# Kernel optimization log

Measured on AMD Instinct MI355X. Metric: run time of the kernel, lower is better.

Reference implementation:

```python
import jax, jax.numpy as jnp
import numpy as np

P = 8192      # num_pois
U = 4096      # num_users
E = 4096      # num directed hyperedges
D = 128       # emb_dim
B = 1024      # batch of user indices
T_UP = 1.0    # args.t1
T_GEO = 1.0   # args.t2
T_P2P = 1.0   # args.t3
ALPHA = 0.8   # constant alpha in Geo_ODEFunc


def setup_inputs() -> dict:
    key = jax.random.key(0)
    ks = jax.random.split(key, 13)
    return {
        "poi_emb_weight": jax.random.normal(ks[0], (P + 1, D), jnp.float32) * 0.02,
        "w_gate_geo": jax.random.normal(ks[1], (D, D), jnp.float32) * 0.05,
        "b_gate_geo": jax.random.normal(ks[2], (1, D), jnp.float32) * 0.05,
        "w_gate_seq": jax.random.normal(ks[3], (D, D), jnp.float32) * 0.05,
        "b_gate_seq": jax.random.normal(ks[4], (1, D), jnp.float32) * 0.05,
        "w_gate_col": jax.random.normal(ks[5], (D, D), jnp.float32) * 0.05,
        "b_gate_col": jax.random.normal(ks[6], (1, D), jnp.float32) * 0.05,
        "HG_up": jax.random.uniform(ks[7], (U, P), jnp.float32) * (1.0 / P),
        "HG_pu": jax.random.uniform(ks[8], (P, U), jnp.float32) * (1.0 / U),
        "HG_poi_src": jax.random.uniform(ks[9], (P, E), jnp.float32) * (1.0 / E),
        "HG_poi_tar": jax.random.uniform(ks[10], (E, P), jnp.float32) * (1.0 / P),
        "poi_geo_graph": jax.random.uniform(ks[11], (P, P), jnp.float32) * (1.0 / P),
        "user_idx": jax.random.randint(ks[12], (B,), 0, U, jnp.int32),
    }


def _gate(pe, w, b):
    # pois_embs * sigmoid(pois_embs @ W + b)
    return pe * jax.nn.sigmoid(pe @ w + b)


def reference(poi_emb_weight, w_gate_geo, b_gate_geo, w_gate_seq, b_gate_seq,
              w_gate_col, b_gate_col, HG_up, HG_pu, HG_poi_src, HG_poi_tar,
              poi_geo_graph, user_idx):
    pe = poi_emb_weight[:-1]                      # drop padding row -> [P, D]
    geo_gate = _gate(pe, w_gate_geo, b_gate_geo)
    seq_gate = _gate(pe, w_gate_seq, b_gate_seq)
    col_gate = _gate(pe, w_gate_col, b_gate_col)

    # U2P ODE, single Euler step on t=[0, T_UP]:
    #   f(x) = (HG_pu@HG_up - I)@x + e, e = x0; A@x factored to avoid [P,P].
    x = col_gate
    hg_pois = x + T_UP * (HG_pu @ (HG_up @ x) - x + x)

    # Geo ODE: f(x) = (alpha/2)*G@x - x + e, e = x0, alpha = 0.8.
    g = geo_gate
    geo_pois = g + T_GEO * ((ALPHA / 2.0) * (poi_geo_graph @ g) - g + g)

    # P2P (directed hypergraph) ODE: A = src@tar, f(x) = (A - I)@x + e.
    s = seq_gate
    trans_pois = s + T_P2P * (HG_poi_src @ (HG_poi_tar @ s) - s + s)

    # structural user embeddings, gathered at batch indices
    hg_users = (HG_up @ hg_pois)[user_idx]        # [B, D]
    geo_users = (HG_up @ geo_pois)[user_idx]      # [B, D]

    # [3P + 2B, D]
    return jnp.concatenate([hg_pois, geo_pois, trans_pois, hg_users, geo_users], axis=0)
```

## Files before the change

### kernel.cpp

```cpp
#include <hip/hip_runtime.h>
#include <hip/hip_bf16.h>

#define PP 8192
#define UU 4096
#define EE 4096
#define BB 1024

using f32x4  = __attribute__((ext_vector_type(4))) float;
using u32x4  = __attribute__((ext_vector_type(4))) unsigned int;
using bf16x8 = __attribute__((ext_vector_type(8))) short;
typedef __hip_bfloat16 bf16_t;

__device__ __forceinline__ unsigned cvt2(float a, float b){
  unsigned r;
  asm("v_cvt_pk_bf16_f32 %0, %1, %2" : "=v"(r) : "v"(a), "v"(b));
  return r;
}

__device__ __forceinline__ void gload16(const void* g, void* l){
  __builtin_amdgcn_global_load_lds((const __attribute__((address_space(1))) void*)g,
                                   (__attribute__((address_space(3))) void*)l, 16, 0, 0);
}

struct Job {
  const float*  A;
  const bf16_t* Bt;
  const float*  add;
  const float*  bvec;
  float*        outF;
  bf16_t*       outT;
  int           outTstride;
  float         scale;
  int           K;
  int           nb;
  int           mode;
};

#define BUFB 24576

__global__ __launch_bounds__(256, 2) void gemm_skinny(Job j0, Job j1, Job j2){
  __shared__ char smem[3*BUFB];
  int bid = blockIdx.x;
  Job j = j0;
  if (bid >= j.nb){ bid -= j.nb; j = j1; if (bid >= j.nb){ bid -= j.nb; j = j2; } }
  const int K = j.K;
  const int T = K >> 6;
  const int m0 = bid << 5;
  const int tid = threadIdx.x;
  const int lane = tid & 63;
  const int wid = tid >> 6;
  const int wm = wid >> 1, wk = wid & 1;

  const char* Ab = (const char*)j.A;
  const char* Bb = (const char*)j.Bt;

  size_t a_src[2]; unsigned a_lds[2];
  #pragma unroll
  for (int i = 0; i < 2; ++i){
    int row = wid*8 + i*4 + (lane>>4);
    int sb  = (lane & 15) << 4;
    a_src[i] = (size_t)(m0 + row)*(size_t)K*4 + (size_t)(sb ^ ((row & 15) << 4));
    a_lds[i] = (unsigned)((wid*8 + i*4) * 256);
  }
  size_t b_src[4]; unsigned b_lds[4];
  #pragma unroll
  for (int i = 0; i < 4; ++i){
    int n  = wid*32 + i*8 + (lane>>3);
    int sb = (lane & 7) << 4;
    b_src[i] = (size_t)n*(size_t)K*2 + (size_t)(sb ^ ((n & 7) << 4));
    b_lds[i] = (unsigned)(8192 + (wid*32 + i*8) * 128);
  }

  const int arow = wm*16 + (lane & 15);
  const unsigned acb  = (unsigned)(wk*128 + ((lane>>4) * 32));
  const unsigned aswz = (unsigned)((lane & 15) << 4);
  const unsigned a_rd0 = arow*256 + (acb ^ aswz);
  const unsigned a_rd1 = arow*256 + ((acb + 16) ^ aswz);
  unsigned b_rd[8];
  #pragma unroll
  for (int n0 = 0; n0 < 8; ++n0){
    int n = n0*16 + (lane & 15);
    unsigned c = (unsigned)(wk*64 + ((lane>>4) * 16));
    b_rd[n0] = 8192u + n*128 + (c ^ ((n & 7) << 4));
  }

  const f32x4 fzero = {0.f, 0.f, 0.f, 0.f};
  f32x4 acc[8];
  #pragma unroll
  for (int i = 0; i < 8; ++i) acc[i] = fzero;

  auto STAGE = [&](unsigned bufoff, int t){
    char* l = smem + bufoff;
    size_t ka = (size_t)t * 256;
    size_t kb = (size_t)t * 128;
    #pragma unroll
    for (int i = 0; i < 2; ++i) gload16(Ab + a_src[i] + ka, l + a_lds[i]);
    #pragma unroll
    for (int i = 0; i < 4; ++i) gload16(Bb + b_src[i] + kb, l + b_lds[i]);
  };

  STAGE(0, 0);
  if (T > 1){
    STAGE(BUFB, 1);
    asm volatile("s_waitcnt vmcnt(6)" ::: "memory");
  } else {
    asm volatile("s_waitcnt vmcnt(0)" ::: "memory");
  }
  __builtin_amdgcn_s_barrier();

  for (int t = 0; t < T; ++t){
    char* l = smem + (unsigned)(t % 3) * BUFB;
    if (t + 2 < T) STAGE((unsigned)((t+2) % 3) * BUFB, t + 2);
    f32x4 a0 = *(const f32x4*)(l + a_rd0);
    f32x4 a1 = *(const f32x4*)(l + a_rd1);
    union { bf16x8 v; unsigned u[4]; } af;
    af.u[0] = cvt2(a0.x, a0.y);
    af.u[1] = cvt2(a0.z, a0.w);
    af.u[2] = cvt2(a1.x, a1.y);
    af.u[3] = cvt2(a1.z, a1.w);
    #pragma unroll
    for (int n0 = 0; n0 < 8; ++n0){
      bf16x8 bfr = *(const bf16x8*)(l + b_rd[n0]);
      acc[n0] = __builtin_amdgcn_mfma_f32_16x16x32_bf16(af.v, bfr, acc[n0], 0, 0, 0);
    }
    if (t + 1 < T){
      if (t + 2 < T) asm volatile("s_waitcnt vmcnt(6)" ::: "memory");
      else           asm volatile("s_waitcnt vmcnt(0)" ::: "memory");
      __builtin_amdgcn_s_barrier();
    }
  }

  __syncthreads();
  float* red = (float*)smem;
  if (wk == 1){
    #pragma unroll
    for (int n0 = 0; n0 < 8; ++n0)
      #pragma unroll
      for (int q = 0; q < 4; ++q){
        int row = wm*16 + ((lane>>4)<<2) + q;
        int col = n0*16 + (lane & 15);
        red[row*128 + col] = acc[n0][q];
      }
  }
  __syncthreads();
  if (wk == 0){
    #pragma unroll
    for (int n0 = 0; n0 < 8; ++n0)
      #pragma unroll
      for (int q = 0; q < 4; ++q){
        int row = wm*16 + ((lane>>4)<<2) + q;
        int col = n0*16 + (lane & 15);
        float v = (acc[n0][q] + red[row*128 + col]) * j.scale;
        size_t gp = (size_t)(m0 + row);
        if (j.mode == 1){
          float pe = j.add[gp*128 + col];
          float bb = j.bvec[col];
          v = pe / (1.f + __expf(-(v + bb)));
        } else if (j.add){
          v += j.add[gp*128 + col];
        }
        acc[n0][q] = v;
        if (j.outF) j.outF[gp*128 + col] = v;
      }
  }

  if (j.outT){
    __syncthreads();
    if (wk == 0){
      #pragma unroll
      for (int n0 = 0; n0 < 8; ++n0)
        #pragma unroll
        for (int q = 0; q < 4; ++q){
          int row = wm*16 + ((lane>>4)<<2) + q;
          int col = n0*16 + (lane & 15);
          red[row*128 + col] = acc[n0][q];
        }
    }
    __syncthreads();
    int col = tid & 127, seg = tid >> 7;
    unsigned wrds[8] __attribute__((aligned(16)));
    #pragma unroll
    for (int r = 0; r < 8; ++r){
      float v0 = red[(seg*16 + 2*r    )*128 + col];
      float v1 = red[(seg*16 + 2*r + 1)*128 + col];
      wrds[r] = cvt2(v0, v1);
    }
    bf16_t* dst = j.outT + (size_t)col * (size_t)j.outTstride + (m0 + seg*16);
    *(u32x4*)dst       = *(const u32x4*)&wrds[0];
    *((u32x4*)dst + 1) = *(const u32x4*)&wrds[4];
  }
}

#define GBUFB 40960

__global__ __launch_bounds__(256, 1) void gemm_gather(const float* __restrict__ Aup,
    const int* __restrict__ uidx, const bf16_t* __restrict__ B5t, float* __restrict__ partials){
  __shared__ char smem[3*GBUFB];
  const int bid = blockIdx.x;
  const int mtile = bid & 31, split = bid >> 5;
  const int tid = threadIdx.x, lane = tid & 63, wid = tid >> 6;
  const int wm = wid >> 1, wk = wid & 1;
  const int T = 16;
  const char* Ab = (const char*)Aup;
  const char* Bb = (const char*)B5t;

  size_t a_src[2]; unsigned a_lds[2];
  #pragma unroll
  for (int i = 0; i < 2; ++i){
    int row  = wid*8 + i*4 + (lane>>4);
    int grow = uidx[mtile*32 + row];
    int sb   = (lane & 15) << 4;
    a_src[i] = (size_t)grow*(size_t)(PP*4) + (size_t)((sb ^ ((row & 15) << 4)) + split*4096);
    a_lds[i] = (unsigned)((wid*8 + i*4) * 256);
  }
  size_t b_src[8]; unsigned b_lds[8];
  #pragma unroll
  for (int i = 0; i < 8; ++i){
    int n  = wid*64 + i*8 + (lane>>3);
    int sb = (lane & 7) << 4;
    b_src[i] = (size_t)n*(size_t)(PP*2) + (size_t)((sb ^ ((n & 7) << 4)) + split*2048);
    b_lds[i] = (unsigned)(8192 + (wid*64 + i*8) * 128);
  }
  const int arow = wm*16 + (lane & 15);
  const unsigned acb  = (unsigned)(wk*128 + ((lane>>4)*32));
  const unsigned aswz = (unsigned)((lane & 15) << 4);
  const unsigned a_rd0 = arow*256 + (acb ^ aswz);
  const unsigned a_rd1 = arow*256 + ((acb + 16) ^ aswz);
  unsigned b_rd[16];
  #pragma unroll
  for (int n0 = 0; n0 < 16; ++n0){
    int n = n0*16 + (lane & 15);
    unsigned c = (unsigned)(wk*64 + ((lane>>4)*16));
    b_rd[n0] = 8192u + n*128 + (c ^ ((n & 7) << 4));
  }
  const f32x4 fzero = {0.f,0.f,0.f,0.f};
  f32x4 acc[16];
  #pragma unroll
  for (int i = 0; i < 16; ++i) acc[i] = fzero;

  auto STAGE = [&](unsigned bufoff, int t){
    char* l = smem + bufoff;
    size_t ka = (size_t)t*256, kb = (size_t)t*128;
    #pragma unroll
    for (int i = 0; i < 2; ++i) gload16(Ab + a_src[i] + ka, l + a_lds[i]);
    #pragma unroll
    for (int i = 0; i < 8; ++i) gload16(Bb + b_src[i] + kb, l + b_lds[i]);
  };
  STAGE(0, 0);
  STAGE(GBUFB, 1);
  asm volatile("s_waitcnt vmcnt(10)" ::: "memory");
  __builtin_amdgcn_s_barrier();
  for (int t = 0; t < T; ++t){
    char* l = smem + (unsigned)(t % 3) * GBUFB;
    if (t + 2 < T) STAGE((unsigned)((t+2)%3)*GBUFB, t+2);
    f32x4 a0 = *(const f32x4*)(l + a_rd0);
    f32x4 a1 = *(const f32x4*)(l + a_rd1);
    union { bf16x8 v; unsigned u[4]; } af;
    af.u[0] = cvt2(a0.x, a0.y);
    af.u[1] = cvt2(a0.z, a0.w);
    af.u[2] = cvt2(a1.x, a1.y);
    af.u[3] = cvt2(a1.z, a1.w);
    #pragma unroll
    for (int n0 = 0; n0 < 16; ++n0){
      bf16x8 bfr = *(const bf16x8*)(l + b_rd[n0]);
      acc[n0] = __builtin_amdgcn_mfma_f32_16x16x32_bf16(af.v, bfr, acc[n0], 0,0,0);
    }
    if (t + 1 < T){
      if (t + 2 < T) asm volatile("s_waitcnt vmcnt(10)" ::: "memory");
      else           asm volatile("s_waitcnt vmcnt(0)" ::: "memory");
      __builtin_amdgcn_s_barrier();
    }
  }
  __syncthreads();
  float* red = (float*)smem;
  if (wk == 1){
    #pragma unroll
    for (int n0 = 0; n0 < 16; ++n0)
      #pragma unroll
      for (int q = 0; q < 4; ++q){
        int row = wm*16 + ((lane>>4)<<2) + q;
        int col = n0*16 + (lane & 15);
        red[row*256 + col] = acc[n0][q];
      }
  }
  __syncthreads();
  if (wk == 0){
    #pragma unroll
    for (int n0 = 0; n0 < 16; ++n0)
      #pragma unroll
      for (int q = 0; q < 4; ++q){
        int row = wm*16 + ((lane>>4)<<2) + q;
        int col = n0*16 + (lane & 15);
        float v = acc[n0][q] + red[row*256 + col];
        partials[((size_t)split*1024 + mtile*32 + row)*256 + col] = v;
      }
  }
}

__global__ void prep_wt(const float* w0, const float* w1, const float* w2,
                        bf16_t* o0, bf16_t* o1, bf16_t* o2){
  const float* w = (blockIdx.x == 0) ? w0 : (blockIdx.x == 1) ? w1 : w2;
  bf16_t*      o = (blockIdx.x == 0) ? o0 : (blockIdx.x == 1) ? o1 : o2;
  int tid = threadIdx.x;
  int n = tid >> 1, h = tid & 1;
  unsigned wr[32] __attribute__((aligned(16)));
  #pragma unroll
  for (int r = 0; r < 32; ++r){
    float v0 = w[(h*64 + 2*r    )*128 + n];
    float v1 = w[(h*64 + 2*r + 1)*128 + n];
    wr[r] = cvt2(v0, v1);
  }
  u32x4* dst = (u32x4*)(o + n*128 + h*64);
  #pragma unroll
  for (int i = 0; i < 8; ++i) dst[i] = *(const u32x4*)&wr[i*4];
}

__global__ void reduce_users(const float* __restrict__ partials, float* __restrict__ out){
  int idx = blockIdx.x * 256 + threadIdx.x;
  int b = idx >> 8, n = idx & 255;
  float s = 0.f;
  #pragma unroll
  for (int k = 0; k < 8; ++k) s += partials[((size_t)k*1024 + b)*256 + n];
  if (n < 128) out[((size_t)(3*PP) + b)*128 + n]           = s;
  else         out[((size_t)(3*PP) + BB + b)*128 + (n-128)] = s;
}

extern "C" void kernel_launch(void* const* d_in, const int* in_sizes, int n_in,
                              void* d_out, int out_size, void* d_ws, size_t ws_size,
                              hipStream_t stream){
  const float* pe   = (const float*)d_in[0];
  const float* wgeo = (const float*)d_in[1];
  const float* bgeo = (const float*)d_in[2];
  const float* wseq = (const float*)d_in[3];
  const float* bseq = (const float*)d_in[4];
  const float* wcol = (const float*)d_in[5];
  const float* bcol = (const float*)d_in[6];
  const float* hup  = (const float*)d_in[7];
  const float* hpu  = (const float*)d_in[8];
  const float* hsrc = (const float*)d_in[9];
  const float* htar = (const float*)d_in[10];
  const float* geo  = (const float*)d_in[11];
  const int*   uidx = (const int*)d_in[12];
  float* out = (float*)d_out;

  char* w = (char*)d_ws;
  const size_t MB = 1024*1024;
  float*  x_f32 = (float*)(w);
  float*  g_f32 = (float*)(w + 4*MB);
  float*  s_f32 = (float*)(w + 8*MB);
  bf16_t* xT    = (bf16_t*)(w + 12*MB);
  bf16_t* gT    = (bf16_t*)(w + 14*MB);
  bf16_t* sT    = (bf16_t*)(w + 16*MB);
  bf16_t* upT   = (bf16_t*)(w + 18*MB);
  bf16_t* tarT  = (bf16_t*)(w + 19*MB);
  bf16_t* b5t   = (bf16_t*)(w + 20*MB);
  bf16_t* wtg   = (bf16_t*)(w + 24*MB);
  bf16_t* wts   = (bf16_t*)(w + 24*MB + 32768);
  bf16_t* wtc   = (bf16_t*)(w + 24*MB + 65536);
  float*  parts = (float*)(w + 25*MB);

  prep_wt<<<3, 256, 0, stream>>>(wgeo, wseq, wcol, wtg, wts, wtc);

  Job jg{pe, wtg, pe, bgeo, g_f32, gT, PP, 1.f, 128, 256, 1};
  Job js{pe, wts, pe, bseq, s_f32, sT, PP, 1.f, 128, 256, 1};
  Job jc{pe, wtc, pe, bcol, x_f32, xT, PP, 1.f, 128, 256, 1};
  gemm_skinny<<<768, 256, 0, stream>>>(jg, js, jc);

  Job j1 {hup,  xT, nullptr, nullptr, nullptr,               upT,                     UU, 1.f,  PP, 128, 0};
  Job j3 {geo,  gT, g_f32,   nullptr, out + (size_t)PP*128,  b5t + (size_t)128*PP,    PP, 0.4f, PP, 256, 0};
  Job j4a{htar, sT, nullptr, nullptr, nullptr,               tarT,                    EE, 1.f,  PP, 128, 0};
  gemm_skinny<<<512, 256, 0, stream>>>(j1, j3, j4a);

  Job j2 {hpu,  upT,  x_f32, nullptr, out,                     b5t,     PP, 1.f, UU, 256, 0};
  Job j4b{hsrc, tarT, s_f32, nullptr, out + (size_t)2*PP*128,  nullptr, 0,  1.f, EE, 256, 0};
  Job jd = j4b; jd.nb = 0;
  gemm_skinny<<<512, 256, 0, stream>>>(j2, j4b, jd);

  gemm_gather<<<256, 256, 0, stream>>>(hup, uidx, b5t, parts);
  reduce_users<<<1024, 256, 0, stream>>>(parts, out);
}
```

Baseline: 286.6 us.

## Double skinny GEMM block to 512 threads, splitting N across wave pairs

Changes gemm_skinny from 256 to 512 threads per block. The 8 waves are split by M, K-half and N-half, so each wave holds 4 accumulator tiles instead of 8 and issues fewer global-to-LDS loads per stage. The vmcnt waits and the transposed bf16 store are adjusted to match. The A-swizzle read uses arow instead of lane, which is equivalent here, in both kernels. The aim is more waves in flight to hide memory latency on these bandwidth-bound skinny GEMMs, at the cost of more barrier participants and higher launch-bounds occupancy demands against 72KB of LDS per block.

New measurement: 274.3 us. -4.3%, faster.

```diff
diff --git a/kernel.cpp b/kernel.cpp
--- a/kernel.cpp
+++ b/kernel.cpp
@@ -38,7 +38,7 @@
 
 #define BUFB 24576
 
-__global__ __launch_bounds__(256, 2) void gemm_skinny(Job j0, Job j1, Job j2){
+__global__ __launch_bounds__(512, 4) void gemm_skinny(Job j0, Job j1, Job j2){
   __shared__ char smem[3*BUFB];
   int bid = blockIdx.x;
   Job j = j0;
@@ -49,60 +49,60 @@
   const int tid = threadIdx.x;
   const int lane = tid & 63;
   const int wid = tid >> 6;
-  const int wm = wid >> 1, wk = wid & 1;
+  const int wn = wid & 1, wk = (wid >> 1) & 1, wm = wid >> 2;
 
   const char* Ab = (const char*)j.A;
   const char* Bb = (const char*)j.Bt;
 
-  size_t a_src[2]; unsigned a_lds[2];
+  size_t a_src; unsigned a_lds;
+  {
+    int L = wid;
+    int row = L*4 + (lane>>4);
+    int sb  = (lane & 15) << 4;
+    a_src = (size_t)(m0 + row)*(size_t)K*4 + (size_t)(sb ^ ((row & 15) << 4));
+    a_lds = (unsigned)(L * 1024);
+  }
+  size_t b_src[2]; unsigned b_lds[2];
   #pragma unroll
   for (int i = 0; i < 2; ++i){
-    int row = wid*8 + i*4 + (lane>>4);
-    int sb  = (lane & 15) << 4;
-    a_src[i] = (size_t)(m0 + row)*(size_t)K*4 + (size_t)(sb ^ ((row & 15) << 4));
-    a_lds[i] = (unsigned)((wid*8 + i*4) * 256);
-  }
-  size_t b_src[4]; unsigned b_lds[4];
-  #pragma unroll
-  for (int i = 0; i < 4; ++i){
-    int n  = wid*32 + i*8 + (lane>>3);
+    int L = wid*2 + i;
+    int n  = L*8 + (lane>>3);
     int sb = (lane & 7) << 4;
     b_src[i] = (size_t)n*(size_t)K*2 + (size_t)(sb ^ ((n & 7) << 4));
-    b_lds[i] = (unsigned)(8192 + (wid*32 + i*8) * 128);
+    b_lds[i] = (unsigned)(8192 + L * 1024);
   }
 
   const int arow = wm*16 + (lane & 15);
   const unsigned acb  = (unsigned)(wk*128 + ((lane>>4) * 32));
-  const unsigned aswz = (unsigned)((lane & 15) << 4);
+  const unsigned aswz = (unsigned)((arow & 15) << 4);
   const unsigned a_rd0 = arow*256 + (acb ^ aswz);
   const unsigned a_rd1 = arow*256 + ((acb + 16) ^ aswz);
-  unsigned b_rd[8];
-  #pragma unroll
-  for (int n0 = 0; n0 < 8; ++n0){
-    int n = n0*16 + (lane & 15);
+  unsigned b_rd[4];
+  #pragma unroll
+  for (int n0 = 0; n0 < 4; ++n0){
+    int n = wn*64 + n0*16 + (lane & 15);
     unsigned c = (unsigned)(wk*64 + ((lane>>4) * 16));
     b_rd[n0] = 8192u + n*128 + (c ^ ((n & 7) << 4));
   }
 
   const f32x4 fzero = {0.f, 0.f, 0.f, 0.f};
-  f32x4 acc[8];
-  #pragma unroll
-  for (int i = 0; i < 8; ++i) acc[i] = fzero;
+  f32x4 acc[4];
+  #pragma unroll
+  for (int i = 0; i < 4; ++i) acc[i] = fzero;
 
   auto STAGE = [&](unsigned bufoff, int t){
     char* l = smem + bufoff;
     size_t ka = (size_t)t * 256;
     size_t kb = (size_t)t * 128;
-    #pragma unroll
-    for (int i = 0; i < 2; ++i) gload16(Ab + a_src[i] + ka, l + a_lds[i]);
-    #pragma unroll
-    for (int i = 0; i < 4; ++i) gload16(Bb + b_src[i] + kb, l + b_lds[i]);
+    gload16(Ab + a_src + ka, l + a_lds);
+    #pragma unroll
+    for (int i = 0; i < 2; ++i) gload16(Bb + b_src[i] + kb, l + b_lds[i]);
   };
 
   STAGE(0, 0);
   if (T > 1){
     STAGE(BUFB, 1);
-    asm volatile("s_waitcnt vmcnt(6)" ::: "memory");
+    asm volatile("s_waitcnt vmcnt(3)" ::: "memory");
   } else {
     asm volatile("s_waitcnt vmcnt(0)" ::: "memory");
   }
@@ -119,12 +119,12 @@
     af.u[2] = cvt2(a1.x, a1.y);
     af.u[3] = cvt2(a1.z, a1.w);
     #pragma unroll
-    for (int n0 = 0; n0 < 8; ++n0){
+    for (int n0 = 0; n0 < 4; ++n0){
       bf16x8 bfr = *(const bf16x8*)(l + b_rd[n0]);
       acc[n0] = __builtin_amdgcn_mfma_f32_16x16x32_bf16(af.v, bfr, acc[n0], 0, 0, 0);
     }
     if (t + 1 < T){
-      if (t + 2 < T) asm volatile("s_waitcnt vmcnt(6)" ::: "memory");
+      if (t + 2 < T) asm volatile("s_waitcnt vmcnt(3)" ::: "memory");
       else           asm volatile("s_waitcnt vmcnt(0)" ::: "memory");
       __builtin_amdgcn_s_barrier();
     }
@@ -134,22 +134,22 @@
   float* red = (float*)smem;
   if (wk == 1){
     #pragma unroll
-    for (int n0 = 0; n0 < 8; ++n0)
+    for (int n0 = 0; n0 < 4; ++n0)
       #pragma unroll
       for (int q = 0; q < 4; ++q){
         int row = wm*16 + ((lane>>4)<<2) + q;
-        int col = n0*16 + (lane & 15);
+        int col = wn*64 + n0*16 + (lane & 15);
         red[row*128 + col] = acc[n0][q];
       }
   }
   __syncthreads();
   if (wk == 0){
     #pragma unroll
-    for (int n0 = 0; n0 < 8; ++n0)
+    for (int n0 = 0; n0 < 4; ++n0)
       #pragma unroll
       for (int q = 0; q < 4; ++q){
         int row = wm*16 + ((lane>>4)<<2) + q;
-        int col = n0*16 + (lane & 15);
+        int col = wn*64 + n0*16 + (lane & 15);
         float v = (acc[n0][q] + red[row*128 + col]) * j.scale;
         size_t gp = (size_t)(m0 + row);
         if (j.mode == 1){
@@ -168,26 +168,25 @@
     __syncthreads();
     if (wk == 0){
       #pragma unroll
-      for (int n0 = 0; n0 < 8; ++n0)
+      for (int n0 = 0; n0 < 4; ++n0)
         #pragma unroll
         for (int q = 0; q < 4; ++q){
           int row = wm*16 + ((lane>>4)<<2) + q;
-          int col = n0*16 + (lane & 15);
+          int col = wn*64 + n0*16 + (lane & 15);
           red[row*128 + col] = acc[n0][q];
         }
     }
     __syncthreads();
     int col = tid & 127, seg = tid >> 7;
-    unsigned wrds[8] __attribute__((aligned(16)));
-    #pragma unroll
-    for (int r = 0; r < 8; ++r){
-      float v0 = red[(seg*16 + 2*r    )*128 + col];
-      float v1 = red[(seg*16 + 2*r + 1)*128 + col];
+    unsigned wrds[4] __attribute__((aligned(16)));
+    #pragma unroll
+    for (int r = 0; r < 4; ++r){
+      float v0 = red[(seg*8 + 2*r    )*128 + col];
+      float v1 = red[(seg*8 + 2*r + 1)*128 + col];
       wrds[r] = cvt2(v0, v1);
     }
-    bf16_t* dst = j.outT + (size_t)col * (size_t)j.outTstride + (m0 + seg*16);
-    *(u32x4*)dst       = *(const u32x4*)&wrds[0];
-    *((u32x4*)dst + 1) = *(const u32x4*)&wrds[4];
+    bf16_t* dst = j.outT + (size_t)col * (size_t)j.outTstride + (m0 + seg*8);
+    *(u32x4*)dst = *(const u32x4*)&wrds[0];
   }
 }
 
@@ -223,7 +222,7 @@
   }
   const int arow = wm*16 + (lane & 15);
   const unsigned acb  = (unsigned)(wk*128 + ((lane>>4)*32));
-  const unsigned aswz = (unsigned)((lane & 15) << 4);
+  const unsigned aswz = (unsigned)((arow & 15) << 4);
   const unsigned a_rd0 = arow*256 + (acb ^ aswz);
   const unsigned a_rd1 = arow*256 + ((acb + 16) ^ aswz);
   unsigned b_rd[16];
@@ -364,17 +363,17 @@
   Job jg{pe, wtg, pe, bgeo, g_f32, gT, PP, 1.f, 128, 256, 1};
   Job js{pe, wts, pe, bseq, s_f32, sT, PP, 1.f, 128, 256, 1};
   Job jc{pe, wtc, pe, bcol, x_f32, xT, PP, 1.f, 128, 256, 1};
-  gemm_skinny<<<768, 256, 0, stream>>>(jg, js, jc);
+  gemm_skinny<<<768, 512, 0, stream>>>(jg, js, jc);
 
   Job j1 {hup,  xT, nullptr, nullptr, nullptr,               upT,                     UU, 1.f,  PP, 128, 0};
   Job j3 {geo,  gT, g_f32,   nullptr, out + (size_t)PP*128,  b5t + (size_t)128*PP,    PP, 0.4f, PP, 256, 0};
   Job j4a{htar, sT, nullptr, nullptr, nullptr,               tarT,                    EE, 1.f,  PP, 128, 0};
-  gemm_skinny<<<512, 256, 0, stream>>>(j1, j3, j4a);
+  gemm_skinny<<<512, 512, 0, stream>>>(j1, j3, j4a);
 
   Job j2 {hpu,  upT,  x_f32, nullptr, out,                     b5t,     PP, 1.f, UU, 256, 0};
   Job j4b{hsrc, tarT, s_f32, nullptr, out + (size_t)2*PP*128,  nullptr, 0,  1.f, EE, 256, 0};
   Job jd = j4b; jd.nb = 0;
-  gemm_skinny<<<512, 256, 0, stream>>>(j2, j4b, jd);
+  gemm_skinny<<<512, 512, 0, stream>>>(j2, j4b, jd);
 
   gemm_gather<<<256, 256, 0, stream>>>(hup, uidx, b5t, parts);
   reduce_users<<<1024, 256, 0, stream>>>(parts, out);
```

## Use 64-row tiles with 512 threads and a 4-stage LDS pipeline in skinny GEMM

Applied to the files above, without the earlier changes.

The skinny GEMM grows from 32-row tiles on 256 threads to 64-row tiles on 512 threads, with a 4-buffer prefetch ring instead of 3 and half as many blocks. LDS fragment reads become explicit batched ds_read_b128 instructions ahead of the MFMA chain, with barriers moved to the start and end of each iteration. The gather GEMM gets the same batched-read and barrier restructuring, and the epilogue writes results straight into the LDS staging area, dropping one synchronisation pass. The aim is deeper memory-latency hiding and better MFMA issue. The trade-off is 128KB of LDS per block, which limits occupancy to one block per CU and leaves fewer blocks across the GPU.

Measured after the change: 301.3 us. 5.1% more time.

```diff
diff --git a/kernel.cpp b/kernel.cpp
--- a/kernel.cpp
+++ b/kernel.cpp
@@ -36,16 +36,16 @@
   int           mode;
 };
 
-#define BUFB 24576
-
-__global__ __launch_bounds__(256, 2) void gemm_skinny(Job j0, Job j1, Job j2){
-  __shared__ char smem[3*BUFB];
+#define BUFB 32768
+
+__global__ __launch_bounds__(512, 2) void gemm_skinny(Job j0, Job j1, Job j2){
+  __shared__ char smem[4*BUFB];
   int bid = blockIdx.x;
   Job j = j0;
   if (bid >= j.nb){ bid -= j.nb; j = j1; if (bid >= j.nb){ bid -= j.nb; j = j2; } }
   const int K = j.K;
   const int T = K >> 6;
-  const int m0 = bid << 5;
+  const int m0 = bid << 6;
   const int tid = threadIdx.x;
   const int lane = tid & 63;
   const int wid = tid >> 6;
@@ -57,31 +57,33 @@
   size_t a_src[2]; unsigned a_lds[2];
   #pragma unroll
   for (int i = 0; i < 2; ++i){
-    int row = wid*8 + i*4 + (lane>>4);
-    int sb  = (lane & 15) << 4;
+    int L = wid*2 + i;
+    int row = L*4 + (lane>>4);
+    unsigned sb = (lane & 15) << 4;
     a_src[i] = (size_t)(m0 + row)*(size_t)K*4 + (size_t)(sb ^ ((row & 15) << 4));
-    a_lds[i] = (unsigned)((wid*8 + i*4) * 256);
-  }
-  size_t b_src[4]; unsigned b_lds[4];
-  #pragma unroll
-  for (int i = 0; i < 4; ++i){
-    int n  = wid*32 + i*8 + (lane>>3);
-    int sb = (lane & 7) << 4;
+    a_lds[i] = (unsigned)(L * 1024);
+  }
+  size_t b_src[2]; unsigned b_lds[2];
+  #pragma unroll
+  for (int i = 0; i < 2; ++i){
+    int L = wid*2 + i;
+    int n  = L*8 + (lane>>3);
+    unsigned sb = (lane & 7) << 4;
     b_src[i] = (size_t)n*(size_t)K*2 + (size_t)(sb ^ ((n & 7) << 4));
-    b_lds[i] = (unsigned)(8192 + (wid*32 + i*8) * 128);
+    b_lds[i] = (unsigned)(16384 + L * 1024);
   }
 
   const int arow = wm*16 + (lane & 15);
-  const unsigned acb  = (unsigned)(wk*128 + ((lane>>4) * 32));
-  const unsigned aswz = (unsigned)((lane & 15) << 4);
-  const unsigned a_rd0 = arow*256 + (acb ^ aswz);
-  const unsigned a_rd1 = arow*256 + ((acb + 16) ^ aswz);
+  const unsigned kcol = (unsigned)(wk*128 + ((lane>>4) * 32));
+  const unsigned aswz = (unsigned)((arow & 15) << 4);
+  const unsigned a_rd0 = arow*256 + (kcol ^ aswz);
+  const unsigned a_rd1 = arow*256 + ((kcol + 16) ^ aswz);
   unsigned b_rd[8];
   #pragma unroll
   for (int n0 = 0; n0 < 8; ++n0){
     int n = n0*16 + (lane & 15);
     unsigned c = (unsigned)(wk*64 + ((lane>>4) * 16));
-    b_rd[n0] = 8192u + n*128 + (c ^ ((n & 7) << 4));
+    b_rd[n0] = 16384u + n*128 + (c ^ ((n & 7) << 4));
   }
 
   const f32x4 fzero = {0.f, 0.f, 0.f, 0.f};
@@ -89,45 +91,57 @@
   #pragma unroll
   for (int i = 0; i < 8; ++i) acc[i] = fzero;
 
-  auto STAGE = [&](unsigned bufoff, int t){
-    char* l = smem + bufoff;
+  auto STAGE = [&](int t){
+    char* l = smem + (unsigned)(t & 3) * BUFB;
     size_t ka = (size_t)t * 256;
     size_t kb = (size_t)t * 128;
-    #pragma unroll
-    for (int i = 0; i < 2; ++i) gload16(Ab + a_src[i] + ka, l + a_lds[i]);
-    #pragma unroll
-    for (int i = 0; i < 4; ++i) gload16(Bb + b_src[i] + kb, l + b_lds[i]);
+    gload16(Ab + a_src[0] + ka, l + a_lds[0]);
+    gload16(Ab + a_src[1] + ka, l + a_lds[1]);
+    gload16(Bb + b_src[0] + kb, l + b_lds[0]);
+    gload16(Bb + b_src[1] + kb, l + b_lds[1]);
   };
 
-  STAGE(0, 0);
-  if (T > 1){
-    STAGE(BUFB, 1);
-    asm volatile("s_waitcnt vmcnt(6)" ::: "memory");
-  } else {
-    asm volatile("s_waitcnt vmcnt(0)" ::: "memory");
-  }
-  __builtin_amdgcn_s_barrier();
+  STAGE(0);
+  if (T > 1) STAGE(1);
+  if (T > 2) STAGE(2);
 
   for (int t = 0; t < T; ++t){
-    char* l = smem + (unsigned)(t % 3) * BUFB;
-    if (t + 2 < T) STAGE((unsigned)((t+2) % 3) * BUFB, t + 2);
-    f32x4 a0 = *(const f32x4*)(l + a_rd0);
-    f32x4 a1 = *(const f32x4*)(l + a_rd1);
+    if (t + 3 < T){ STAGE(t + 3); asm volatile("s_waitcnt vmcnt(12)" ::: "memory"); }
+    else if (t + 2 < T) asm volatile("s_waitcnt vmcnt(8)" ::: "memory");
+    else if (t + 1 < T) asm volatile("s_waitcnt vmcnt(4)" ::: "memory");
+    else                asm volatile("s_waitcnt vmcnt(0)" ::: "memory");
+    __builtin_amdgcn_s_barrier();
+
+    const unsigned bo = (unsigned)(t & 3) * BUFB;
+    f32x4 a0, a1;
+    asm volatile("ds_read_b128 %0, %1" : "=v"(a0) : "v"(bo + a_rd0));
+    asm volatile("ds_read_b128 %0, %1" : "=v"(a1) : "v"(bo + a_rd1));
+    bf16x8 bfr0, bfr1, bfr2, bfr3, bfr4, bfr5, bfr6, bfr7;
+    asm volatile("ds_read_b128 %0, %1" : "=v"(bfr0) : "v"(bo + b_rd[0]));
+    asm volatile("ds_read_b128 %0, %1" : "=v"(bfr1) : "v"(bo + b_rd[1]));
+    asm volatile("ds_read_b128 %0, %1" : "=v"(bfr2) : "v"(bo + b_rd[2]));
+    asm volatile("ds_read_b128 %0, %1" : "=v"(bfr3) : "v"(bo + b_rd[3]));
+    asm volatile("ds_read_b128 %0, %1" : "=v"(bfr4) : "v"(bo + b_rd[4]));
+    asm volatile("ds_read_b128 %0, %1" : "=v"(bfr5) : "v"(bo + b_rd[5]));
+    asm volatile("ds_read_b128 %0, %1" : "=v"(bfr6) : "v"(bo + b_rd[6]));
+    asm volatile("ds_read_b128 %0, %1" : "=v"(bfr7) : "v"(bo + b_rd[7]));
+    asm volatile("s_waitcnt lgkmcnt(0)" ::: "memory");
+    __builtin_amdgcn_sched_barrier(0);
+
     union { bf16x8 v; unsigned u[4]; } af;
     af.u[0] = cvt2(a0.x, a0.y);
     af.u[1] = cvt2(a0.z, a0.w);
     af.u[2] = cvt2(a1.x, a1.y);
     af.u[3] = cvt2(a1.z, a1.w);
-    #pragma unroll
-    for (int n0 = 0; n0 < 8; ++n0){
-      bf16x8 bfr = *(const bf16x8*)(l + b_rd[n0]);
-      acc[n0] = __builtin_amdgcn_mfma_f32_16x16x32_bf16(af.v, bfr, acc[n0], 0, 0, 0);
-    }
-    if (t + 1 < T){
-      if (t + 2 < T) asm volatile("s_waitcnt vmcnt(6)" ::: "memory");
-      else           asm volatile("s_waitcnt vmcnt(0)" ::: "memory");
-      __builtin_amdgcn_s_barrier();
-    }
+    acc[0] = __builtin_amdgcn_mfma_f32_16x16x32_bf16(af.v, bfr0, acc[0], 0,0,0);
+    acc[1] = __builtin_amdgcn_mfma_f32_16x16x32_bf16(af.v, bfr1, acc[1], 0,0,0);
+    acc[2] = __builtin_amdgcn_mfma_f32_16x16x32_bf16(af.v, bfr2, acc[2], 0,0,0);
+    acc[3] = __builtin_amdgcn_mfma_f32_16x16x32_bf16(af.v, bfr3, acc[3], 0,0,0);
+    acc[4] = __builtin_amdgcn_mfma_f32_16x16x32_bf16(af.v, bfr4, acc[4], 0,0,0);
+    acc[5] = __builtin_amdgcn_mfma_f32_16x16x32_bf16(af.v, bfr5, acc[5], 0,0,0);
+    acc[6] = __builtin_amdgcn_mfma_f32_16x16x32_bf16(af.v, bfr6, acc[6], 0,0,0);
+    acc[7] = __builtin_amdgcn_mfma_f32_16x16x32_bf16(af.v, bfr7, acc[7], 0,0,0);
+    __builtin_amdgcn_s_barrier();
   }
 
   __syncthreads();
@@ -159,23 +173,12 @@
         } else if (j.add){
           v += j.add[gp*128 + col];
         }
-        acc[n0][q] = v;
         if (j.outF) j.outF[gp*128 + col] = v;
+        red[row*128 + col] = v;
       }
   }
 
   if (j.outT){
-    __syncthreads();
-    if (wk == 0){
-      #pragma unroll
-      for (int n0 = 0; n0 < 8; ++n0)
-        #pragma unroll
-        for (int q = 0; q < 4; ++q){
-          int row = wm*16 + ((lane>>4)<<2) + q;
-          int col = n0*16 + (lane & 15);
-          red[row*128 + col] = acc[n0][q];
-        }
-    }
     __syncthreads();
     int col = tid & 127, seg = tid >> 7;
     unsigned wrds[8] __attribute__((aligned(16)));
@@ -209,7 +212,7 @@
   for (int i = 0; i < 2; ++i){
     int row  = wid*8 + i*4 + (lane>>4);
     int grow = uidx[mtile*32 + row];
-    int sb   = (lane & 15) << 4;
+    unsigned sb = (lane & 15) << 4;
     a_src[i] = (size_t)grow*(size_t)(PP*4) + (size_t)((sb ^ ((row & 15) << 4)) + split*4096);
     a_lds[i] = (unsigned)((wid*8 + i*4) * 256);
   }
@@ -217,13 +220,13 @@
   #pragma unroll
   for (int i = 0; i < 8; ++i){
     int n  = wid*64 + i*8 + (lane>>3);
-    int sb = (lane & 7) << 4;
+    unsigned sb = (lane & 7) << 4;
     b_src[i] = (size_t)n*(size_t)(PP*2) + (size_t)((sb ^ ((n & 7) << 4)) + split*2048);
     b_lds[i] = (unsigned)(8192 + (wid*64 + i*8) * 128);
   }
   const int arow = wm*16 + (lane & 15);
   const unsigned acb  = (unsigned)(wk*128 + ((lane>>4)*32));
-  const unsigned aswz = (unsigned)((lane & 15) << 4);
+  const unsigned aswz = (unsigned)((arow & 15) << 4);
   const unsigned a_rd0 = arow*256 + (acb ^ aswz);
   const unsigned a_rd1 = arow*256 + ((acb + 16) ^ aswz);
   unsigned b_rd[16];
@@ -238,38 +241,69 @@
   #pragma unroll
   for (int i = 0; i < 16; ++i) acc[i] = fzero;
 
-  auto STAGE = [&](unsigned bufoff, int t){
-    char* l = smem + bufoff;
+  auto STAGE = [&](int t){
+    char* l = smem + (unsigned)(t % 3) * GBUFB;
     size_t ka = (size_t)t*256, kb = (size_t)t*128;
     #pragma unroll
     for (int i = 0; i < 2; ++i) gload16(Ab + a_src[i] + ka, l + a_lds[i]);
     #pragma unroll
     for (int i = 0; i < 8; ++i) gload16(Bb + b_src[i] + kb, l + b_lds[i]);
   };
-  STAGE(0, 0);
-  STAGE(GBUFB, 1);
-  asm volatile("s_waitcnt vmcnt(10)" ::: "memory");
-  __builtin_amdgcn_s_barrier();
+  STAGE(0);
+  STAGE(1);
   for (int t = 0; t < T; ++t){
-    char* l = smem + (unsigned)(t % 3) * GBUFB;
-    if (t + 2 < T) STAGE((unsigned)((t+2)%3)*GBUFB, t+2);
-    f32x4 a0 = *(const f32x4*)(l + a_rd0);
-    f32x4 a1 = *(const f32x4*)(l + a_rd1);
+    if (t + 2 < T){ STAGE(t + 2); asm volatile("s_waitcnt vmcnt(20)" ::: "memory"); }
+    else if (t + 1 < T) asm volatile("s_waitcnt vmcnt(10)" ::: "memory");
+    else                asm volatile("s_waitcnt vmcnt(0)" ::: "memory");
+    __builtin_amdgcn_s_barrier();
+
+    const unsigned bo = (unsigned)(t % 3) * GBUFB;
+    f32x4 a0, a1;
+    asm volatile("ds_read_b128 %0, %1" : "=v"(a0) : "v"(bo + a_rd0));
+    asm volatile("ds_read_b128 %0, %1" : "=v"(a1) : "v"(bo + a_rd1));
+    bf16x8 bf0, bf1, bf2, bf3, bf4, bf5, bf6, bf7;
+    bf16x8 bf8, bf9, bf10, bf11, bf12, bf13, bf14, bf15;
+    asm volatile("ds_read_b128 %0, %1" : "=v"(bf0)  : "v"(bo + b_rd[0]));
+    asm volatile("ds_read_b128 %0, %1" : "=v"(bf1)  : "v"(bo + b_rd[1]));
+    asm volatile("ds_read_b128 %0, %1" : "=v"(bf2)  : "v"(bo + b_rd[2]));
+    asm volatile("ds_read_b128 %0, %1" : "=v"(bf3)  : "v"(bo + b_rd[3]));
+    asm volatile("ds_read_b128 %0, %1" : "=v"(bf4)  : "v"(bo + b_rd[4]));
+    asm volatile("ds_read_b128 %0, %1" : "=v"(bf5)  : "v"(bo + b_rd[5]));
+    asm volatile("ds_read_b128 %0, %1" : "=v"(bf6)  : "v"(bo + b_rd[6]));
+    asm volatile("ds_read_b128 %0, %1" : "=v"(bf7)  : "v"(bo + b_rd[7]));
+    asm volatile("ds_read_b128 %0, %1" : "=v"(bf8)  : "v"(bo + b_rd[8]));
+    asm volatile("ds_read_b128 %0, %1" : "=v"(bf9)  : "v"(bo + b_rd[9]));
+    asm volatile("ds_read_b128 %0, %1" : "=v"(bf10) : "v"(bo + b_rd[10]));
+    asm volatile("ds_read_b128 %0, %1" : "=v"(bf11) : "v"(bo + b_rd[11]));
+    asm volatile("ds_read_b128 %0, %1" : "=v"(bf12) : "v"(bo + b_rd[12]));
+    asm volatile("ds_read_b128 %0, %1" : "=v"(bf13) : "v"(bo + b_rd[13]));
+    asm volatile("ds_read_b128 %0, %1" : "=v"(bf14) : "v"(bo + b_rd[14]));
+    asm volatile("ds_read_b128 %0, %1" : "=v"(bf15) : "v"(bo + b_rd[15]));
+    asm volatile("s_waitcnt lgkmcnt(0)" ::: "memory");
+    __builtin_amdgcn_sched_barrier(0);
+
     union { bf16x8 v; unsigned u[4]; } af;
     af.u[0] = cvt2(a0.x, a0.y);
     af.u[1] = cvt2(a0.z, a0.w);
     af.u[2] = cvt2(a1.x, a1.y);
     af.u[3] = cvt2(a1.z, a1.w);
-    #pragma unroll
-    for (int n0 = 0; n0 < 16; ++n0){
-      bf16x8 bfr = *(const bf16x8*)(l + b_rd[n0]);
-      acc[n0] = __builtin_amdgcn_mfma_f32_16x16x32_bf16(af.v, bfr, acc[n0], 0,0,0);
-    }
-    if (t + 1 < T){
-      if (t + 2 < T) asm volatile("s_waitcnt vmcnt(10)" ::: "memory");
-      else           asm volatile("s_waitcnt vmcnt(0)" ::: "memory");
-      __builtin_amdgcn_s_barrier();
-    }
+    acc[0]  = __builtin_amdgcn_mfma_f32_16x16x32_bf16(af.v, bf0,  acc[0],  0,0,0);
+    acc[1]  = __builtin_amdgcn_mfma_f32_16x16x32_bf16(af.v, bf1,  acc[1],  0,0,0);
+    acc[2]  = __builtin_amdgcn_mfma_f32_16x16x32_bf16(af.v, bf2,  acc[2],  0,0,0);
+    acc[3]  = __builtin_amdgcn_mfma_f32_16x16x32_bf16(af.v, bf3,  acc[3],  0,0,0);
+    acc[4]  = __builtin_amdgcn_mfma_f32_16x16x32_bf16(af.v, bf4,  acc[4],  0,0,0);
+    acc[5]  = __builtin_amdgcn_mfma_f32_16x16x32_bf16(af.v, bf5,  acc[5],  0,0,0);
+    acc[6]  = __builtin_amdgcn_mfma_f32_16x16x32_bf16(af.v, bf6,  acc[6],  0,0,0);
+    acc[7]  = __builtin_amdgcn_mfma_f32_16x16x32_bf16(af.v, bf7,  acc[7],  0,0,0);
+    acc[8]  = __builtin_amdgcn_mfma_f32_16x16x32_bf16(af.v, bf8,  acc[8],  0,0,0);
+    acc[9]  = __builtin_amdgcn_mfma_f32_16x16x32_bf16(af.v, bf9,  acc[9],  0,0,0);
+    acc[10] = __builtin_amdgcn_mfma_f32_16x16x32_bf16(af.v, bf10, acc[10], 0,0,0);
+    acc[11] = __builtin_amdgcn_mfma_f32_16x16x32_bf16(af.v, bf11, acc[11], 0,0,0);
+    acc[12] = __builtin_amdgcn_mfma_f32_16x16x32_bf16(af.v, bf12, acc[12], 0,0,0);
+    acc[13] = __builtin_amdgcn_mfma_f32_16x16x32_bf16(af.v, bf13, acc[13], 0,0,0);
+    acc[14] = __builtin_amdgcn_mfma_f32_16x16x32_bf16(af.v, bf14, acc[14], 0,0,0);
+    acc[15] = __builtin_amdgcn_mfma_f32_16x16x32_bf16(af.v, bf15, acc[15], 0,0,0);
+    __builtin_amdgcn_s_barrier();
   }
   __syncthreads();
   float* red = (float*)smem;
@@ -361,20 +395,20 @@
 
   prep_wt<<<3, 256, 0, stream>>>(wgeo, wseq, wcol, wtg, wts, wtc);
 
-  Job jg{pe, wtg, pe, bgeo, g_f32, gT, PP, 1.f, 128, 256, 1};
-  Job js{pe, wts, pe, bseq, s_f32, sT, PP, 1.f, 128, 256, 1};
-  Job jc{pe, wtc, pe, bcol, x_f32, xT, PP, 1.f, 128, 256, 1};
-  gemm_skinny<<<768, 256, 0, stream>>>(jg, js, jc);
-
-  Job j1 {hup,  xT, nullptr, nullptr, nullptr,               upT,                     UU, 1.f,  PP, 128, 0};
-  Job j3 {geo,  gT, g_f32,   nullptr, out + (size_t)PP*128,  b5t + (size_t)128*PP,    PP, 0.4f, PP, 256, 0};
-  Job j4a{htar, sT, nullptr, nullptr, nullptr,               tarT,                    EE, 1.f,  PP, 128, 0};
-  gemm_skinny<<<512, 256, 0, stream>>>(j1, j3, j4a);
-
-  Job j2 {hpu,  upT,  x_f32, nullptr, out,                     b5t,     PP, 1.f, UU, 256, 0};
-  Job j4b{hsrc, tarT, s_f32, nullptr, out + (size_t)2*PP*128,  nullptr, 0,  1.f, EE, 256, 0};
+  Job jg{pe, wtg, pe, bgeo, g_f32, gT, PP, 1.f, 128, 128, 1};
+  Job js{pe, wts, pe, bseq, s_f32, sT, PP, 1.f, 128, 128, 1};
+  Job jc{pe, wtc, pe, bcol, x_f32, xT, PP, 1.f, 128, 128, 1};
+  gemm_skinny<<<384, 512, 0, stream>>>(jg, js, jc);
+
+  Job j1 {hup,  xT, nullptr, nullptr, nullptr,               upT,                  UU, 1.f,  PP, 64,  0};
+  Job j3 {geo,  gT, g_f32,   nullptr, out + (size_t)PP*128,  b5t + (size_t)128*PP, PP, 0.4f, PP, 128, 0};
+  Job j4a{htar, sT, nullptr, nullptr, nullptr,               tarT,                 EE, 1.f,  PP, 64,  0};
+  gemm_skinny<<<256, 512, 0, stream>>>(j1, j3, j4a);
+
+  Job j2 {hpu,  upT,  x_f32, nullptr, out,                     b5t,     PP, 1.f, UU, 128, 0};
+  Job j4b{hsrc, tarT, s_f32, nullptr, out + (size_t)2*PP*128,  nullptr, 0,  1.f, EE, 128, 0};
   Job jd = j4b; jd.nb = 0;
-  gemm_skinny<<<512, 256, 0, stream>>>(j2, j4b, jd);
+  gemm_skinny<<<256, 512, 0, stream>>>(j2, j4b, jd);
 
   gemm_gather<<<256, 256, 0, stream>>>(hup, uidx, b5t, parts);
   reduce_users<<<1024, 256, 0, stream>>>(parts, out);
```

## Load A operand straight to registers and unroll skinny GEMM pipeline by two

Applied to the files above, without the earlier changes.

The skinny GEMM no longer stages the fp32 A tile through LDS. Each lane loads its own A fragment directly into registers with inline global_load_dwordx4, which shrinks the per-buffer LDS to the B tile only. The smaller LDS footprint lets launch bounds rise to 3 blocks per CU. The main loop is manually unrolled by two with even/odd register buffers, explicit ds_read batches and sched_barriers, to overlap global loads with MFMA work. The gather kernel's A swizzle is changed to use the row index rather than the lane, and the direct A loads give up LDS coalescing, so each lane reads strided 32-byte chunks.

New measurement: 297.4 us. 3.7% more time.

```diff
diff --git a/kernel.cpp b/kernel.cpp
--- a/kernel.cpp
+++ b/kernel.cpp
@@ -36,9 +36,15 @@
   int           mode;
 };
 
-#define BUFB 24576
-
-__global__ __launch_bounds__(256, 2) void gemm_skinny(Job j0, Job j1, Job j2){
+#define BUFB 16384
+
+#define ALOAD(d0, d1) do { \
+    asm volatile("global_load_dwordx4 %0, %2, off\n\t" \
+                 "global_load_dwordx4 %1, %2, off offset:16" \
+      : "=&v"(d0), "=&v"(d1) : "v"(aaddr) : "memory"); \
+    aaddr += 256; } while(0)
+
+__global__ __launch_bounds__(256, 3) void gemm_skinny(Job j0, Job j1, Job j2){
   __shared__ char smem[3*BUFB];
   int bid = blockIdx.x;
   Job j = j0;
@@ -51,83 +57,116 @@
   const int wid = tid >> 6;
   const int wm = wid >> 1, wk = wid & 1;
 
-  const char* Ab = (const char*)j.A;
   const char* Bb = (const char*)j.Bt;
 
-  size_t a_src[2]; unsigned a_lds[2];
-  #pragma unroll
-  for (int i = 0; i < 2; ++i){
-    int row = wid*8 + i*4 + (lane>>4);
-    int sb  = (lane & 15) << 4;
-    a_src[i] = (size_t)(m0 + row)*(size_t)K*4 + (size_t)(sb ^ ((row & 15) << 4));
-    a_lds[i] = (unsigned)((wid*8 + i*4) * 256);
-  }
   size_t b_src[4]; unsigned b_lds[4];
   #pragma unroll
   for (int i = 0; i < 4; ++i){
-    int n  = wid*32 + i*8 + (lane>>3);
-    int sb = (lane & 7) << 4;
+    int L = wid*4 + i;
+    int n = L*8 + (lane>>3);
+    unsigned sb = (lane & 7) << 4;
     b_src[i] = (size_t)n*(size_t)K*2 + (size_t)(sb ^ ((n & 7) << 4));
-    b_lds[i] = (unsigned)(8192 + (wid*32 + i*8) * 128);
-  }
-
-  const int arow = wm*16 + (lane & 15);
-  const unsigned acb  = (unsigned)(wk*128 + ((lane>>4) * 32));
-  const unsigned aswz = (unsigned)((lane & 15) << 4);
-  const unsigned a_rd0 = arow*256 + (acb ^ aswz);
-  const unsigned a_rd1 = arow*256 + ((acb + 16) ^ aswz);
+    b_lds[i] = (unsigned)(L * 1024);
+  }
   unsigned b_rd[8];
   #pragma unroll
   for (int n0 = 0; n0 < 8; ++n0){
     int n = n0*16 + (lane & 15);
     unsigned c = (unsigned)(wk*64 + ((lane>>4) * 16));
-    b_rd[n0] = 8192u + n*128 + (c ^ ((n & 7) << 4));
-  }
+    b_rd[n0] = (unsigned)(n*128) + (c ^ ((n & 7) << 4));
+  }
+  const char* aaddr = (const char*)j.A
+      + (size_t)(m0 + wm*16 + (lane & 15)) * (size_t)K * 4
+      + (unsigned)(wk*128 + ((lane>>4) << 5));
 
   const f32x4 fzero = {0.f, 0.f, 0.f, 0.f};
   f32x4 acc[8];
   #pragma unroll
   for (int i = 0; i < 8; ++i) acc[i] = fzero;
 
-  auto STAGE = [&](unsigned bufoff, int t){
-    char* l = smem + bufoff;
-    size_t ka = (size_t)t * 256;
+  auto STAGE = [&](int buf, int t){
+    char* l = smem + (unsigned)buf * BUFB;
     size_t kb = (size_t)t * 128;
-    #pragma unroll
-    for (int i = 0; i < 2; ++i) gload16(Ab + a_src[i] + ka, l + a_lds[i]);
     #pragma unroll
     for (int i = 0; i < 4; ++i) gload16(Bb + b_src[i] + kb, l + b_lds[i]);
   };
 
-  STAGE(0, 0);
-  if (T > 1){
-    STAGE(BUFB, 1);
+  f32x4 aE0, aE1, aO0, aO1;
+  STAGE(0, 0); ALOAD(aE0, aE1);
+  STAGE(1, 1); ALOAD(aO0, aO1);
+
+  int rbuf = 0;
+  for (int t = 0; t < T; t += 2){
     asm volatile("s_waitcnt vmcnt(6)" ::: "memory");
-  } else {
-    asm volatile("s_waitcnt vmcnt(0)" ::: "memory");
-  }
-  __builtin_amdgcn_s_barrier();
-
-  for (int t = 0; t < T; ++t){
-    char* l = smem + (unsigned)(t % 3) * BUFB;
-    if (t + 2 < T) STAGE((unsigned)((t+2) % 3) * BUFB, t + 2);
-    f32x4 a0 = *(const f32x4*)(l + a_rd0);
-    f32x4 a1 = *(const f32x4*)(l + a_rd1);
-    union { bf16x8 v; unsigned u[4]; } af;
-    af.u[0] = cvt2(a0.x, a0.y);
-    af.u[1] = cvt2(a0.z, a0.w);
-    af.u[2] = cvt2(a1.x, a1.y);
-    af.u[3] = cvt2(a1.z, a1.w);
-    #pragma unroll
-    for (int n0 = 0; n0 < 8; ++n0){
-      bf16x8 bfr = *(const bf16x8*)(l + b_rd[n0]);
-      acc[n0] = __builtin_amdgcn_mfma_f32_16x16x32_bf16(af.v, bfr, acc[n0], 0, 0, 0);
-    }
-    if (t + 1 < T){
-      if (t + 2 < T) asm volatile("s_waitcnt vmcnt(6)" ::: "memory");
-      else           asm volatile("s_waitcnt vmcnt(0)" ::: "memory");
+    __builtin_amdgcn_sched_barrier(0);
+    {
+      union { bf16x8 v; unsigned u[4]; } af;
+      af.u[0] = cvt2(aE0.x, aE0.y);
+      af.u[1] = cvt2(aE0.z, aE0.w);
+      af.u[2] = cvt2(aE1.x, aE1.y);
+      af.u[3] = cvt2(aE1.z, aE1.w);
+      int sbuf = rbuf + 2; if (sbuf >= 3) sbuf -= 3;
+      if (t + 2 < T){ STAGE(sbuf, t + 2); ALOAD(aE0, aE1); }
       __builtin_amdgcn_s_barrier();
-    }
+      const unsigned bo = (unsigned)rbuf * BUFB;
+      bf16x8 b0,b1,b2,b3,b4,b5,b6,b7;
+      asm volatile("ds_read_b128 %0, %1" : "=v"(b0) : "v"(bo + b_rd[0]));
+      asm volatile("ds_read_b128 %0, %1" : "=v"(b1) : "v"(bo + b_rd[1]));
+      asm volatile("ds_read_b128 %0, %1" : "=v"(b2) : "v"(bo + b_rd[2]));
+      asm volatile("ds_read_b128 %0, %1" : "=v"(b3) : "v"(bo + b_rd[3]));
+      asm volatile("ds_read_b128 %0, %1" : "=v"(b4) : "v"(bo + b_rd[4]));
+      asm volatile("ds_read_b128 %0, %1" : "=v"(b5) : "v"(bo + b_rd[5]));
+      asm volatile("ds_read_b128 %0, %1" : "=v"(b6) : "v"(bo + b_rd[6]));
+      asm volatile("ds_read_b128 %0, %1" : "=v"(b7) : "v"(bo + b_rd[7]));
+      asm volatile("s_waitcnt lgkmcnt(0)" ::: "memory");
+      __builtin_amdgcn_sched_barrier(0);
+      acc[0] = __builtin_amdgcn_mfma_f32_16x16x32_bf16(af.v, b0, acc[0], 0,0,0);
+      acc[1] = __builtin_amdgcn_mfma_f32_16x16x32_bf16(af.v, b1, acc[1], 0,0,0);
+      acc[2] = __builtin_amdgcn_mfma_f32_16x16x32_bf16(af.v, b2, acc[2], 0,0,0);
+      acc[3] = __builtin_amdgcn_mfma_f32_16x16x32_bf16(af.v, b3, acc[3], 0,0,0);
+      acc[4] = __builtin_amdgcn_mfma_f32_16x16x32_bf16(af.v, b4, acc[4], 0,0,0);
+      acc[5] = __builtin_amdgcn_mfma_f32_16x16x32_bf16(af.v, b5, acc[5], 0,0,0);
+      acc[6] = __builtin_amdgcn_mfma_f32_16x16x32_bf16(af.v, b6, acc[6], 0,0,0);
+      acc[7] = __builtin_amdgcn_mfma_f32_16x16x32_bf16(af.v, b7, acc[7], 0,0,0);
+      __builtin_amdgcn_s_barrier();
+    }
+    if (++rbuf == 3) rbuf = 0;
+
+    if (t + 2 < T) asm volatile("s_waitcnt vmcnt(6)" ::: "memory");
+    else           asm volatile("s_waitcnt vmcnt(0)" ::: "memory");
+    __builtin_amdgcn_sched_barrier(0);
+    {
+      union { bf16x8 v; unsigned u[4]; } af;
+      af.u[0] = cvt2(aO0.x, aO0.y);
+      af.u[1] = cvt2(aO0.z, aO0.w);
+      af.u[2] = cvt2(aO1.x, aO1.y);
+      af.u[3] = cvt2(aO1.z, aO1.w);
+      int sbuf = rbuf + 2; if (sbuf >= 3) sbuf -= 3;
+      if (t + 3 < T){ STAGE(sbuf, t + 3); ALOAD(aO0, aO1); }
+      __builtin_amdgcn_s_barrier();
+      const unsigned bo = (unsigned)rbuf * BUFB;
+      bf16x8 b0,b1,b2,b3,b4,b5,b6,b7;
+      asm volatile("ds_read_b128 %0, %1" : "=v"(b0) : "v"(bo + b_rd[0]));
+      asm volatile("ds_read_b128 %0, %1" : "=v"(b1) : "v"(bo + b_rd[1]));
+      asm volatile("ds_read_b128 %0, %1" : "=v"(b2) : "v"(bo + b_rd[2]));
+      asm volatile("ds_read_b128 %0, %1" : "=v"(b3) : "v"(bo + b_rd[3]));
+      asm volatile("ds_read_b128 %0, %1" : "=v"(b4) : "v"(bo + b_rd[4]));
+      asm volatile("ds_read_b128 %0, %1" : "=v"(b5) : "v"(bo + b_rd[5]));
+      asm volatile("ds_read_b128 %0, %1" : "=v"(b6) : "v"(bo + b_rd[6]));
+      asm volatile("ds_read_b128 %0, %1" : "=v"(b7) : "v"(bo + b_rd[7]));
+      asm volatile("s_waitcnt lgkmcnt(0)" ::: "memory");
+      __builtin_amdgcn_sched_barrier(0);
+      acc[0] = __builtin_amdgcn_mfma_f32_16x16x32_bf16(af.v, b0, acc[0], 0,0,0);
+      acc[1] = __builtin_amdgcn_mfma_f32_16x16x32_bf16(af.v, b1, acc[1], 0,0,0);
+      acc[2] = __builtin_amdgcn_mfma_f32_16x16x32_bf16(af.v, b2, acc[2], 0,0,0);
+      acc[3] = __builtin_amdgcn_mfma_f32_16x16x32_bf16(af.v, b3, acc[3], 0,0,0);
+      acc[4] = __builtin_amdgcn_mfma_f32_16x16x32_bf16(af.v, b4, acc[4], 0,0,0);
+      acc[5] = __builtin_amdgcn_mfma_f32_16x16x32_bf16(af.v, b5, acc[5], 0,0,0);
+      acc[6] = __builtin_amdgcn_mfma_f32_16x16x32_bf16(af.v, b6, acc[6], 0,0,0);
+      acc[7] = __builtin_amdgcn_mfma_f32_16x16x32_bf16(af.v, b7, acc[7], 0,0,0);
+      __builtin_amdgcn_s_barrier();
+    }
+    if (++rbuf == 3) rbuf = 0;
   }
 
   __syncthreads();
@@ -209,7 +248,7 @@
   for (int i = 0; i < 2; ++i){
     int row  = wid*8 + i*4 + (lane>>4);
     int grow = uidx[mtile*32 + row];
-    int sb   = (lane & 15) << 4;
+    unsigned sb = (lane & 15) << 4;
     a_src[i] = (size_t)grow*(size_t)(PP*4) + (size_t)((sb ^ ((row & 15) << 4)) + split*4096);
     a_lds[i] = (unsigned)((wid*8 + i*4) * 256);
   }
@@ -217,13 +256,13 @@
   #pragma unroll
   for (int i = 0; i < 8; ++i){
     int n  = wid*64 + i*8 + (lane>>3);
-    int sb = (lane & 7) << 4;
+    unsigned sb = (lane & 7) << 4;
     b_src[i] = (size_t)n*(size_t)(PP*2) + (size_t)((sb ^ ((n & 7) << 4)) + split*2048);
     b_lds[i] = (unsigned)(8192 + (wid*64 + i*8) * 128);
   }
   const int arow = wm*16 + (lane & 15);
   const unsigned acb  = (unsigned)(wk*128 + ((lane>>4)*32));
-  const unsigned aswz = (unsigned)((lane & 15) << 4);
+  const unsigned aswz = (unsigned)((arow & 15) << 4);
   const unsigned a_rd0 = arow*256 + (acb ^ aswz);
   const unsigned a_rd1 = arow*256 + ((acb + 16) ^ aswz);
   unsigned b_rd[16];
@@ -366,9 +405,9 @@
   Job jc{pe, wtc, pe, bcol, x_f32, xT, PP, 1.f, 128, 256, 1};
   gemm_skinny<<<768, 256, 0, stream>>>(jg, js, jc);
 
-  Job j1 {hup,  xT, nullptr, nullptr, nullptr,               upT,                     UU, 1.f,  PP, 128, 0};
-  Job j3 {geo,  gT, g_f32,   nullptr, out + (size_t)PP*128,  b5t + (size_t)128*PP,    PP, 0.4f, PP, 256, 0};
-  Job j4a{htar, sT, nullptr, nullptr, nullptr,               tarT,                    EE, 1.f,  PP, 128, 0};
+  Job j1 {hup,  xT, nullptr, nullptr, nullptr,               upT,                  UU, 1.f,  PP, 128, 0};
+  Job j3 {geo,  gT, g_f32,   nullptr, out + (size_t)PP*128,  b5t + (size_t)128*PP, PP, 0.4f, PP, 256, 0};
+  Job j4a{htar, sT, nullptr, nullptr, nullptr,               tarT,                 EE, 1.f,  PP, 128, 0};
   gemm_skinny<<<512, 256, 0, stream>>>(j1, j3, j4a);
 
   Job j2 {hpu,  upT,  x_f32, nullptr, out,                     b5t,     PP, 1.f, UU, 256, 0};
```
